# Kernel optimization log

Hardware: AMD Instinct MI355X
Metric: run time of the kernel (lower is better)

The kernel has to match this reference:

```python
import jax, jax.numpy as jnp
import numpy as np

EPS = 1e-5  # torch GroupNorm default


def setup_inputs() -> dict:
    key = jax.random.key(0)
    ks = jax.random.split(key, 7)
    B, H, W, C = 8, 64, 64, 64
    x = jax.random.normal(ks[0], (B, H, W, C), dtype=jnp.float32)
    temb = jax.random.normal(ks[1], (B, 256), dtype=jnp.float32)
    scale = 0.02
    Wq = jax.random.normal(ks[2], (C, C), dtype=jnp.float32) * scale
    Wk = jax.random.normal(ks[3], (C, C), dtype=jnp.float32) * scale
    Wv = jax.random.normal(ks[4], (C, C), dtype=jnp.float32) * scale
    Wo = jax.random.normal(ks[5], (C, C), dtype=jnp.float32) * scale
    z = jnp.zeros((C,), dtype=jnp.float32)
    return {"x": x, "temb": temb, "Wq": Wq, "bq": z, "Wk": Wk, "bk": z,
            "Wv": Wv, "bv": z, "Wo": Wo, "bo": z}


def reference(x, temb, Wq, bq, Wk, bk, Wv, bv, Wo, bo):
    # x: [B, H, W, C] channels-last. temb is accepted but unused (as in source).
    B, H, W, C = x.shape
    S = H * W
    # normalize(): freshly-built GroupNorm(num_groups=1) with identity affine
    # -> standardize over all non-batch dims.
    mu = jnp.mean(x, axis=(1, 2, 3), keepdims=True)
    var = jnp.var(x, axis=(1, 2, 3), keepdims=True)
    h = (x - mu) * jax.lax.rsqrt(var + EPS)
    hf = h.reshape(B, S, C)
    q = hf @ Wq.T + bq  # [B, S, C]
    k = hf @ Wk.T + bk
    v = hf @ Wv.T + bv
    # full (S x S) score matrix, scaled by C^-0.5, naive softmax
    w = jnp.einsum('bsc,btc->bst', q, k) * (C ** -0.5)
    w = jax.nn.softmax(w, axis=-1)
    o = jnp.einsum('bst,btc->bsc', w, v)  # [B, S, C]
    o = o @ Wo.T + bo
    return x + o.reshape(B, H, W, C)
```

## Files before the change

kernel.cpp:

```cpp
#include <hip/hip_runtime.h>
#include <hip/hip_bf16.h>
#include <math.h>

#define B_ 8
#define S_ 4096
#define C_ 64
#define EPSV 1e-5f

using floatx4 = __attribute__((ext_vector_type(4))) float;
using bf16x8  = __attribute__((ext_vector_type(8))) short;
using bf16x4  = __attribute__((ext_vector_type(4))) short;

typedef __attribute__((address_space(3))) unsigned int       as3_u32;
typedef __attribute__((address_space(1))) const unsigned int as1_u32;

__device__ __forceinline__ short f2bf(float f) {
    unsigned u = __builtin_bit_cast(unsigned, f);
    u = u + 0x7fffu + ((u >> 16) & 1u);
    return (short)(u >> 16);
}

__device__ __forceinline__ float bf2f(short s) {
    return __builtin_bit_cast(float, ((unsigned)(unsigned short)s) << 16);
}

__device__ __forceinline__ unsigned cvt_pk_bf16(float lo, float hi) {
    unsigned r;
    asm volatile("v_cvt_pk_bf16_f32 %0, %1, %2" : "=v"(r) : "v"(lo), "v"(hi));
    return r;
}

__device__ __forceinline__ floatx4 mfma_16x16x16_bf16(bf16x4 a, bf16x4 b, floatx4 c) {
#if __has_builtin(__builtin_amdgcn_mfma_f32_16x16x16bf16_1k)
    return __builtin_amdgcn_mfma_f32_16x16x16bf16_1k(a, b, c, 0, 0, 0);
#else
    asm("v_mfma_f32_16x16x16_bf16 %0, %1, %2, %0" : "+v"(c) : "v"(a), "v"(b));
    return c;
#endif
}

__device__ __forceinline__ bf16x8 ld_w_frag(const float* __restrict__ W, int n, int kk, int g, int c) {
    const float* p = W + (16 * n + c) * C_ + 32 * kk + 8 * g;
    bf16x8 r;
#pragma unroll
    for (int j = 0; j < 8; ++j) r[j] = f2bf(p[j]);
    return r;
}

__global__ __launch_bounds__(256) void stats1_kernel(const float* __restrict__ x,
                                                     float* __restrict__ partial) {
    int b = blockIdx.x >> 5, chunk = blockIdx.x & 31;
    const float4* xb = (const float4*)x + (size_t)b * 65536 + chunk * 2048;
    float s = 0.f, ss = 0.f;
#pragma unroll
    for (int i = 0; i < 8; ++i) {
        float4 v = xb[threadIdx.x + i * 256];
        s  += v.x + v.y + v.z + v.w;
        ss += v.x * v.x + v.y * v.y + v.z * v.z + v.w * v.w;
    }
    for (int off = 32; off > 0; off >>= 1) {
        s  += __shfl_down(s, off);
        ss += __shfl_down(ss, off);
    }
    __shared__ float sm[4], ssm[4];
    int wid = threadIdx.x >> 6, lane = threadIdx.x & 63;
    if (lane == 0) { sm[wid] = s; ssm[wid] = ss; }
    __syncthreads();
    if (threadIdx.x == 0) {
        partial[blockIdx.x * 2]     = sm[0] + sm[1] + sm[2] + sm[3];
        partial[blockIdx.x * 2 + 1] = ssm[0] + ssm[1] + ssm[2] + ssm[3];
    }
}

__global__ __launch_bounds__(512) void stats2_kernel(const float* __restrict__ partial,
                                                     float* __restrict__ stats) {
    int w = threadIdx.x >> 6, lane = threadIdx.x & 63;
    float s = 0.f, ss = 0.f;
    if (lane < 32) {
        s  = partial[(w * 32 + lane) * 2];
        ss = partial[(w * 32 + lane) * 2 + 1];
    }
    for (int off = 16; off > 0; off >>= 1) {
        s  += __shfl_down(s, off);
        ss += __shfl_down(ss, off);
    }
    if (lane == 0) {
        const float invN = 1.0f / (float)(S_ * C_);
        float mu  = s * invN;
        float var = ss * invN - mu * mu;
        stats[w * 2]     = mu;
        stats[w * 2 + 1] = rsqrtf(var + EPSV);
    }
}

__global__ __launch_bounds__(256) void proj_kernel(
    const float* __restrict__ x,
    const float* __restrict__ Wq, const float* __restrict__ bq,
    const float* __restrict__ Wk, const float* __restrict__ bk,
    const float* __restrict__ Wv, const float* __restrict__ bv,
    const float* __restrict__ stats,
    short* __restrict__ qo, char* __restrict__ kws, char* __restrict__ vws) {
    __shared__ char hbuf[64 * 128];

    int b  = blockIdx.x >> 6;
    int t_ = blockIdx.x & 63;
    int s0 = t_ * 64;
    float mu = stats[b * 2], rs = stats[b * 2 + 1];
    const float* xt = x + ((size_t)b * S_ + s0) * C_;
    int t = threadIdx.x;

#pragma unroll
    for (int i = 0; i < 4; ++i) {
        int fi  = t + 256 * i;
        int row = fi >> 4;
        int c4  = fi & 15;
        float4 v = *(const float4*)(xt + row * C_ + c4 * 4);
        unsigned lo = (unsigned)(unsigned short)f2bf((v.x - mu) * rs) |
                      ((unsigned)(unsigned short)f2bf((v.y - mu) * rs) << 16);
        unsigned hi = (unsigned)(unsigned short)f2bf((v.z - mu) * rs) |
                      ((unsigned)(unsigned short)f2bf((v.w - mu) * rs) << 16);
        int off = row * 128 + c4 * 8;
        off ^= (row & 7) << 4;
        *(uint2*)(hbuf + off) = make_uint2(lo, hi);
    }
    __syncthreads();

    int lane = t & 63, w = t >> 6;
    int g = lane >> 4, c = lane & 15;

    auto ld_h = [&](int row, int kcol) -> bf16x8 {
        int off = row * 128 + kcol * 2;
        off ^= (row & 7) << 4;
        return *(const bf16x8*)(hbuf + off);
    };

    bf16x8 ha[2];
    ha[0] = ld_h(16 * w + c, 8 * g);
    ha[1] = ld_h(16 * w + c, 32 + 8 * g);

    const float QSC = 0.125f * 1.44269504088896340736f;

#pragma unroll
    for (int n = 0; n < 4; ++n) {
        floatx4 aq = {0.f, 0.f, 0.f, 0.f}, ak = {0.f, 0.f, 0.f, 0.f};
#pragma unroll
        for (int kk = 0; kk < 2; ++kk) {
            bf16x8 wq = ld_w_frag(Wq, n, kk, g, c);
            bf16x8 wk = ld_w_frag(Wk, n, kk, g, c);
            aq = __builtin_amdgcn_mfma_f32_16x16x32_bf16(ha[kk], wq, aq, 0, 0, 0);
            ak = __builtin_amdgcn_mfma_f32_16x16x32_bf16(ha[kk], wk, ak, 0, 0, 0);
        }
        float bqv = bq[16 * n + c], bkv = bk[16 * n + c];
#pragma unroll
        for (int r = 0; r < 4; ++r) {
            int rr = 16 * w + 4 * g + r;
            qo[((size_t)b * S_ + s0 + rr) * C_ + 16 * n + c] = f2bf((aq[r] + bqv) * QSC);
            int r32 = rr & 31;
            size_t tb = ((size_t)b * 128 + 2 * t_ + (rr >> 5)) * 4096;
            int koff = (r32 * 128 + (16 * n + c) * 2) ^ ((r32 & 7) << 4);
            *(short*)(kws + tb + koff) = f2bf(ak[r] + bkv);
        }
    }

    bf16x8 wv[2];
    wv[0] = ld_w_frag(Wv, w, 0, g, c);
    wv[1] = ld_w_frag(Wv, w, 1, g, c);
    float bvr[4];
#pragma unroll
    for (int r = 0; r < 4; ++r) bvr[r] = bv[16 * w + 4 * g + r];

#pragma unroll
    for (int n = 0; n < 4; ++n) {
        floatx4 av = {0.f, 0.f, 0.f, 0.f};
#pragma unroll
        for (int kk = 0; kk < 2; ++kk) {
            bf16x8 hb = ld_h(16 * n + c, 32 * kk + 8 * g);
            av = __builtin_amdgcn_mfma_f32_16x16x32_bf16(wv[kk], hb, av, 0, 0, 0);
        }
        int u   = 16 * n + c;
        int u32 = u & 31;
        size_t tb = ((size_t)b * 128 + 2 * t_ + (u >> 5)) * 4096;
#pragma unroll
        for (int r = 0; r < 4; ++r) {
            int rr = 16 * w + 4 * g + r;
            int voff = (rr * 64 + u32 * 2) ^ ((rr & 7) << 3);
            *(short*)(vws + tb + voff) = f2bf(av[r] + bvr[r]);
        }
    }
}

__global__ __launch_bounds__(256, 8) void flash_kernel(
    const short* __restrict__ qm, const char* __restrict__ kws, const char* __restrict__ vws,
    short* __restrict__ Opart, float2* __restrict__ mlpart) {
    __shared__ char lds[16384];

    int bid = blockIdx.x;
    int logical = (bid & 7) * 256 + (bid >> 3);
    int b = logical >> 8;
    int rest = logical & 255;
    int q0 = (rest >> 2) * 64;
    int quarter = rest & 3;
    int t = threadIdx.x;
    int lane = t & 63, w = t >> 6;
    int g = lane >> 4, c = lane & 15;
    int qw = q0 + 16 * w;

    const char* kbase = kws + (size_t)b * 128 * 4096;
    const char* vbase = vws + (size_t)b * 128 * 4096;
    const short* qp = qm + (size_t)b * S_ * C_;

    bf16x8 bqf[2];
    bqf[0] = *(const bf16x8*)(qp + (qw + c) * C_ + 8 * g);
    bqf[1] = *(const bf16x8*)(qp + (qw + c) * C_ + 32 + 8 * g);

    floatx4 oacc[4];
#pragma unroll
    for (int n = 0; n < 4; ++n) oacc[n] = (floatx4){0.f, 0.f, 0.f, 0.f};
    float m = -__builtin_inff(), lsum = 0.f;

    const int xmask  = (c & 7) << 4;
    const int vxmask = (c & 7) << 3;

    auto STAGE = [&](int bi, int tt) {
        const char* gk = kbase + (size_t)tt * 4096 + t * 16;
        const char* gv = vbase + (size_t)tt * 4096 + t * 16;
        char* lk = lds +        bi * 4096 + t * 16;
        char* lv = lds + 8192 + bi * 4096 + t * 16;
        __builtin_amdgcn_global_load_lds((as1_u32*)gk, (as3_u32*)lk, 16, 0, 0);
        __builtin_amdgcn_global_load_lds((as1_u32*)gv, (as3_u32*)lv, 16, 0, 0);
    };

    auto ld_k = [&](const char* buf, int s, int colb) -> bf16x8 {
        return *(const bf16x8*)(buf + s * 2048 + c * 128 + (colb ^ xmask));
    };
    auto ld_v = [&](const char* buf, int mi, int s) -> bf16x4 {
        return *(const bf16x4*)(buf + mi * 1024 + c * 64 + ((32 * s + 8 * g) ^ vxmask));
    };

    auto COMPUTE = [&](int bi) {
        const char* kbuf = lds +        bi * 4096;
        const char* vbuf = lds + 8192 + bi * 4096;
        floatx4 st[2];
        __builtin_amdgcn_s_setprio(1);
#pragma unroll
        for (int s = 0; s < 2; ++s) {
            st[s] = (floatx4){0.f, 0.f, 0.f, 0.f};
#pragma unroll
            for (int kk = 0; kk < 2; ++kk) {
                bf16x8 ak = ld_k(kbuf, s, 64 * kk + 16 * g);
                st[s] = __builtin_amdgcn_mfma_f32_16x16x32_bf16(ak, bqf[kk], st[s], 0, 0, 0);
            }
        }
        __builtin_amdgcn_s_setprio(0);
        float mt = st[0][0];
#pragma unroll
        for (int s = 0; s < 2; ++s)
#pragma unroll
            for (int r = 0; r < 4; ++r) mt = fmaxf(mt, st[s][r]);
        mt = fmaxf(mt, __shfl_xor(mt, 16));
        mt = fmaxf(mt, __shfl_xor(mt, 32));
        if (!__all(mt - m <= 8.0f)) {
            float mnew  = fmaxf(m, mt);
            float alpha = __builtin_amdgcn_exp2f(m - mnew);
            lsum *= alpha;
            m = mnew;
#pragma unroll
            for (int n = 0; n < 4; ++n) oacc[n] *= alpha;
        }
        bf16x4 pb[2];
        float psum = 0.f;
#pragma unroll
        for (int s = 0; s < 2; ++s) {
            float e0 = __builtin_amdgcn_exp2f(st[s][0] - m);
            float e1 = __builtin_amdgcn_exp2f(st[s][1] - m);
            float e2 = __builtin_amdgcn_exp2f(st[s][2] - m);
            float e3 = __builtin_amdgcn_exp2f(st[s][3] - m);
            psum += (e0 + e1) + (e2 + e3);
            uint2 u = make_uint2(cvt_pk_bf16(e0, e1), cvt_pk_bf16(e2, e3));
            pb[s] = __builtin_bit_cast(bf16x4, u);
        }
        lsum += psum;
        __builtin_amdgcn_s_setprio(1);
#pragma unroll
        for (int s = 0; s < 2; ++s) {
#pragma unroll
            for (int mi = 0; mi < 4; ++mi) {
                bf16x4 av = ld_v(vbuf, mi, s);
                oacc[mi] = mfma_16x16x16_bf16(av, pb[s], oacc[mi]);
            }
        }
        __builtin_amdgcn_s_setprio(0);
    };

    const int base = quarter * 32;
    STAGE(0, base);
    __syncthreads();
    for (int r = 0; r < 32; r += 2) {
        STAGE(1, base + r + 1);
        COMPUTE(0);
        __syncthreads();
        if (r + 2 < 32) STAGE(0, base + r + 2);
        COMPUTE(1);
        __syncthreads();
    }

    lsum += __shfl_xor(lsum, 16);
    lsum += __shfl_xor(lsum, 32);

    size_t prow = (size_t)(quarter * 8 + b) * S_ + q0;
    if (lane < 16)
        mlpart[prow + 16 * w + lane] = make_float2(m, lsum);

    short* op = Opart + (prow + 16 * w + c) * C_;
#pragma unroll
    for (int mi = 0; mi < 4; ++mi) {
        uint2 u = make_uint2(cvt_pk_bf16(oacc[mi][0], oacc[mi][1]),
                             cvt_pk_bf16(oacc[mi][2], oacc[mi][3]));
        *(uint2*)(op + 16 * mi + 4 * g) = u;
    }
}

__global__ __launch_bounds__(256) void combine_kernel(
    const short* __restrict__ Opart, const float2* __restrict__ mlpart,
    const float* __restrict__ Wo, const float* __restrict__ bo,
    const float* __restrict__ x, float* __restrict__ out) {
    __shared__ char obuf[8192];

    int bid = blockIdx.x;
    int logical = (bid & 7) * 64 + (bid >> 3);
    int b = logical >> 6;
    int q0 = (logical & 63) * 64;
    int t = threadIdx.x;
    int lane = t & 63, w = t >> 6;
    int g = lane >> 4, c = lane & 15;

    const short*  P[4];
    const float2* ml[4];
#pragma unroll
    for (int h = 0; h < 4; ++h) {
        P[h]  = Opart  + ((size_t)(h * 8 + b) * S_ + q0) * C_;
        ml[h] = mlpart + (size_t)(h * 8 + b) * S_ + q0;
    }

#pragma unroll
    for (int i = 0; i < 16; ++i) {
        int idx = t + 256 * i;
        int q = idx >> 6, ch = idx & 63;
        float2 a0 = ml[0][q], a1 = ml[1][q], a2 = ml[2][q], a3 = ml[3][q];
        float M = fmaxf(fmaxf(a0.x, a1.x), fmaxf(a2.x, a3.x));
        float s0 = __builtin_amdgcn_exp2f(a0.x - M);
        float s1 = __builtin_amdgcn_exp2f(a1.x - M);
        float s2 = __builtin_amdgcn_exp2f(a2.x - M);
        float s3 = __builtin_amdgcn_exp2f(a3.x - M);
        float L  = a0.y * s0 + a1.y * s1 + a2.y * s2 + a3.y * s3;
        float o  = (bf2f(P[0][q * 64 + ch]) * s0 + bf2f(P[1][q * 64 + ch]) * s1 +
                    bf2f(P[2][q * 64 + ch]) * s2 + bf2f(P[3][q * 64 + ch]) * s3) / L;
        int off = (q * 128 + ch * 2) ^ ((q & 7) << 4);
        *(short*)(obuf + off) = f2bf(o);
    }
    __syncthreads();

    bf16x8 ao[2];
    {
        int row = 16 * w + c;
        int off0 = (row * 128 + (8 * g) * 2)      ^ ((row & 7) << 4);
        int off1 = (row * 128 + (32 + 8 * g) * 2) ^ ((row & 7) << 4);
        ao[0] = *(const bf16x8*)(obuf + off0);
        ao[1] = *(const bf16x8*)(obuf + off1);
    }
#pragma unroll
    for (int n = 0; n < 4; ++n) {
        floatx4 a = {0.f, 0.f, 0.f, 0.f};
#pragma unroll
        for (int kk = 0; kk < 2; ++kk) {
            bf16x8 bw = ld_w_frag(Wo, n, kk, g, c);
            a = __builtin_amdgcn_mfma_f32_16x16x32_bf16(ao[kk], bw, a, 0, 0, 0);
        }
        float bov = bo[16 * n + c];
#pragma unroll
        for (int r = 0; r < 4; ++r) {
            int srow = q0 + 16 * w + 4 * g + r;
            size_t idx = ((size_t)b * S_ + srow) * C_ + 16 * n + c;
            out[idx] = x[idx] + bov + a[r];
        }
    }
}

extern "C" void kernel_launch(void* const* d_in, const int* in_sizes, int n_in,
                              void* d_out, int out_size, void* d_ws, size_t ws_size,
                              hipStream_t stream) {
    const float* x  = (const float*)d_in[0];
    const float* Wq = (const float*)d_in[2];
    const float* bq = (const float*)d_in[3];
    const float* Wk = (const float*)d_in[4];
    const float* bk = (const float*)d_in[5];
    const float* Wv = (const float*)d_in[6];
    const float* bv = (const float*)d_in[7];
    const float* Wo = (const float*)d_in[8];
    const float* bo = (const float*)d_in[9];
    float* out = (float*)d_out;

    char* ws = (char*)d_ws;
    float*  partial = (float*)ws;
    float*  stats   = (float*)(ws + 2048);
    short*  q   = (short*)(ws + 4096);
    char*   kt  = (char*)(q + (size_t)B_ * S_ * C_);
    char*   vt  = kt + (size_t)B_ * 128 * 4096;
    short*  op  = (short*)(vt + (size_t)B_ * 128 * 4096);
    float2* mlp = (float2*)((char*)op + (size_t)4 * B_ * S_ * C_ * 2);

    stats1_kernel<<<256, 256, 0, stream>>>(x, partial);
    stats2_kernel<<<1, 512, 0, stream>>>(partial, stats);
    proj_kernel<<<B_ * (S_ / 64), 256, 0, stream>>>(x, Wq, bq, Wk, bk, Wv, bv, stats, q, kt, vt);
    flash_kernel<<<B_ * (S_ / 64) * 4, 256, 0, stream>>>(q, kt, vt, op, mlp);
    combine_kernel<<<B_ * (S_ / 64), 256, 0, stream>>>(op, mlp, Wo, bo, x, out);
}
```

Measured before the change: 93.74 us.

## Process two query tiles per wave to reuse staged K/V fragments

Each wave now handles 32 query rows (two 16-row tiles) instead of 16, so every block covers 128 queries and the grid is halved. K and V fragments loaded from LDS are read once into registers and reused for both query tiles, halving LDS reads and global K/V staging per query. The cost is roughly double the accumulator and score registers, with launch bounds lowered to 4 waves per SIMD, which may reduce occupancy and latency hiding.

```diff
diff --git a/kernel.cpp b/kernel.cpp
--- a/kernel.cpp
+++ b/kernel.cpp
@@ -189,34 +189,39 @@
     }
 }
 
-__global__ __launch_bounds__(256, 8) void flash_kernel(
+__global__ __launch_bounds__(256, 4) void flash_kernel(
     const short* __restrict__ qm, const char* __restrict__ kws, const char* __restrict__ vws,
     short* __restrict__ Opart, float2* __restrict__ mlpart) {
     __shared__ char lds[16384];
 
     int bid = blockIdx.x;
-    int logical = (bid & 7) * 256 + (bid >> 3);
-    int b = logical >> 8;
-    int rest = logical & 255;
-    int q0 = (rest >> 2) * 64;
+    int logical = (bid & 7) * 128 + (bid >> 3);
+    int b = logical >> 7;
+    int rest = logical & 127;
+    int q0 = (rest >> 2) * 128;
     int quarter = rest & 3;
     int t = threadIdx.x;
     int lane = t & 63, w = t >> 6;
     int g = lane >> 4, c = lane & 15;
-    int qw = q0 + 16 * w;
+    int qw = q0 + 32 * w;
 
     const char* kbase = kws + (size_t)b * 128 * 4096;
     const char* vbase = vws + (size_t)b * 128 * 4096;
     const short* qp = qm + (size_t)b * S_ * C_;
 
-    bf16x8 bqf[2];
-    bqf[0] = *(const bf16x8*)(qp + (qw + c) * C_ + 8 * g);
-    bqf[1] = *(const bf16x8*)(qp + (qw + c) * C_ + 32 + 8 * g);
-
-    floatx4 oacc[4];
-#pragma unroll
-    for (int n = 0; n < 4; ++n) oacc[n] = (floatx4){0.f, 0.f, 0.f, 0.f};
-    float m = -__builtin_inff(), lsum = 0.f;
+    bf16x8 bqf[2][2];
+#pragma unroll
+    for (int qi = 0; qi < 2; ++qi) {
+        bqf[qi][0] = *(const bf16x8*)(qp + (qw + 16 * qi + c) * C_ + 8 * g);
+        bqf[qi][1] = *(const bf16x8*)(qp + (qw + 16 * qi + c) * C_ + 32 + 8 * g);
+    }
+
+    floatx4 oacc[2][4];
+#pragma unroll
+    for (int qi = 0; qi < 2; ++qi)
+#pragma unroll
+        for (int mi = 0; mi < 4; ++mi) oacc[qi][mi] = (floatx4){0.f, 0.f, 0.f, 0.f};
+    float m[2] = {-__builtin_inff(), -__builtin_inff()}, l[2] = {0.f, 0.f};
 
     const int xmask  = (c & 7) << 4;
     const int vxmask = (c & 7) << 3;
@@ -240,55 +245,74 @@
     auto COMPUTE = [&](int bi) {
         const char* kbuf = lds +        bi * 4096;
         const char* vbuf = lds + 8192 + bi * 4096;
-        floatx4 st[2];
+        bf16x8 ak[2][2];
+#pragma unroll
+        for (int s = 0; s < 2; ++s)
+#pragma unroll
+            for (int kk = 0; kk < 2; ++kk)
+                ak[s][kk] = ld_k(kbuf, s, 64 * kk + 16 * g);
+        floatx4 st[2][2];
         __builtin_amdgcn_s_setprio(1);
 #pragma unroll
-        for (int s = 0; s < 2; ++s) {
-            st[s] = (floatx4){0.f, 0.f, 0.f, 0.f};
-#pragma unroll
-            for (int kk = 0; kk < 2; ++kk) {
-                bf16x8 ak = ld_k(kbuf, s, 64 * kk + 16 * g);
-                st[s] = __builtin_amdgcn_mfma_f32_16x16x32_bf16(ak, bqf[kk], st[s], 0, 0, 0);
+        for (int qi = 0; qi < 2; ++qi)
+#pragma unroll
+            for (int s = 0; s < 2; ++s) {
+                st[qi][s] = (floatx4){0.f, 0.f, 0.f, 0.f};
+                st[qi][s] = __builtin_amdgcn_mfma_f32_16x16x32_bf16(ak[s][0], bqf[qi][0], st[qi][s], 0, 0, 0);
+                st[qi][s] = __builtin_amdgcn_mfma_f32_16x16x32_bf16(ak[s][1], bqf[qi][1], st[qi][s], 0, 0, 0);
             }
-        }
         __builtin_amdgcn_s_setprio(0);
-        float mt = st[0][0];
+        bf16x4 av[2][4];
 #pragma unroll
         for (int s = 0; s < 2; ++s)
 #pragma unroll
-            for (int r = 0; r < 4; ++r) mt = fmaxf(mt, st[s][r]);
-        mt = fmaxf(mt, __shfl_xor(mt, 16));
-        mt = fmaxf(mt, __shfl_xor(mt, 32));
-        if (!__all(mt - m <= 8.0f)) {
-            float mnew  = fmaxf(m, mt);
-            float alpha = __builtin_amdgcn_exp2f(m - mnew);
-            lsum *= alpha;
-            m = mnew;
-#pragma unroll
-            for (int n = 0; n < 4; ++n) oacc[n] *= alpha;
-        }
-        bf16x4 pb[2];
-        float psum = 0.f;
-#pragma unroll
-        for (int s = 0; s < 2; ++s) {
-            float e0 = __builtin_amdgcn_exp2f(st[s][0] - m);
-            float e1 = __builtin_amdgcn_exp2f(st[s][1] - m);
-            float e2 = __builtin_amdgcn_exp2f(st[s][2] - m);
-            float e3 = __builtin_amdgcn_exp2f(st[s][3] - m);
-            psum += (e0 + e1) + (e2 + e3);
-            uint2 u = make_uint2(cvt_pk_bf16(e0, e1), cvt_pk_bf16(e2, e3));
-            pb[s] = __builtin_bit_cast(bf16x4, u);
-        }
-        lsum += psum;
+            for (int mi = 0; mi < 4; ++mi)
+                av[s][mi] = ld_v(vbuf, mi, s);
+        float mt[2], need = -1e30f;
+#pragma unroll
+        for (int qi = 0; qi < 2; ++qi) {
+            float v = fmaxf(fmaxf(st[qi][0][0], st[qi][0][1]), fmaxf(st[qi][0][2], st[qi][0][3]));
+            v = fmaxf(v, fmaxf(fmaxf(st[qi][1][0], st[qi][1][1]), fmaxf(st[qi][1][2], st[qi][1][3])));
+            v = fmaxf(v, __shfl_xor(v, 16));
+            v = fmaxf(v, __shfl_xor(v, 32));
+            mt[qi] = v;
+            need = fmaxf(need, v - m[qi]);
+        }
+        if (!__all(need <= 8.0f)) {
+#pragma unroll
+            for (int qi = 0; qi < 2; ++qi) {
+                float mn = fmaxf(m[qi], mt[qi]);
+                float a  = __builtin_amdgcn_exp2f(m[qi] - mn);
+                m[qi] = mn;
+                l[qi] *= a;
+#pragma unroll
+                for (int mi = 0; mi < 4; ++mi) oacc[qi][mi] *= a;
+            }
+        }
+        bf16x4 pb[2][2];
+#pragma unroll
+        for (int qi = 0; qi < 2; ++qi) {
+            float psum = 0.f;
+#pragma unroll
+            for (int s = 0; s < 2; ++s) {
+                float e0 = __builtin_amdgcn_exp2f(st[qi][s][0] - m[qi]);
+                float e1 = __builtin_amdgcn_exp2f(st[qi][s][1] - m[qi]);
+                float e2 = __builtin_amdgcn_exp2f(st[qi][s][2] - m[qi]);
+                float e3 = __builtin_amdgcn_exp2f(st[qi][s][3] - m[qi]);
+                psum += (e0 + e1) + (e2 + e3);
+                uint2 u = make_uint2(cvt_pk_bf16(e0, e1), cvt_pk_bf16(e2, e3));
+                pb[qi][s] = __builtin_bit_cast(bf16x4, u);
+            }
+            l[qi] += psum;
+        }
         __builtin_amdgcn_s_setprio(1);
 #pragma unroll
-        for (int s = 0; s < 2; ++s) {
-#pragma unroll
-            for (int mi = 0; mi < 4; ++mi) {
-                bf16x4 av = ld_v(vbuf, mi, s);
-                oacc[mi] = mfma_16x16x16_bf16(av, pb[s], oacc[mi]);
-            }
-        }
+        for (int qi = 0; qi < 2; ++qi)
+#pragma unroll
+            for (int s = 0; s < 2; ++s)
+#pragma unroll
+                for (int mi = 0; mi < 4; ++mi)
+                    oacc[qi][mi] = mfma_16x16x16_bf16(av[s][mi], pb[qi][s], oacc[qi][mi]);
         __builtin_amdgcn_s_setprio(0);
     };
 
@@ -304,19 +328,28 @@
         __syncthreads();
     }
 
-    lsum += __shfl_xor(lsum, 16);
-    lsum += __shfl_xor(lsum, 32);
+#pragma unroll
+    for (int qi = 0; qi < 2; ++qi) {
+        l[qi] += __shfl_xor(l[qi], 16);
+        l[qi] += __shfl_xor(l[qi], 32);
+    }
 
     size_t prow = (size_t)(quarter * 8 + b) * S_ + q0;
-    if (lane < 16)
-        mlpart[prow + 16 * w + lane] = make_float2(m, lsum);
-
-    short* op = Opart + (prow + 16 * w + c) * C_;
-#pragma unroll
-    for (int mi = 0; mi < 4; ++mi) {
-        uint2 u = make_uint2(cvt_pk_bf16(oacc[mi][0], oacc[mi][1]),
-                             cvt_pk_bf16(oacc[mi][2], oacc[mi][3]));
-        *(uint2*)(op + 16 * mi + 4 * g) = u;
+    if (lane < 16) {
+#pragma unroll
+        for (int qi = 0; qi < 2; ++qi)
+            mlpart[prow + 32 * w + 16 * qi + lane] = make_float2(m[qi], l[qi]);
+    }
+
+#pragma unroll
+    for (int qi = 0; qi < 2; ++qi) {
+        short* op = Opart + (prow + 32 * w + 16 * qi + c) * C_;
+#pragma unroll
+        for (int mi = 0; mi < 4; ++mi) {
+            uint2 u = make_uint2(cvt_pk_bf16(oacc[qi][mi][0], oacc[qi][mi][1]),
+                                 cvt_pk_bf16(oacc[qi][mi][2], oacc[qi][mi][3]));
+            *(uint2*)(op + 16 * mi + 4 * g) = u;
+        }
     }
 }
 
@@ -412,6 +445,6 @@
     stats1_kernel<<<256, 256, 0, stream>>>(x, partial);
     stats2_kernel<<<1, 512, 0, stream>>>(partial, stats);
     proj_kernel<<<B_ * (S_ / 64), 256, 0, stream>>>(x, Wq, bq, Wk, bk, Wv, bv, stats, q, kt, vt);
-    flash_kernel<<<B_ * (S_ / 64) * 4, 256, 0, stream>>>(q, kt, vt, op, mlp);
+    flash_kernel<<<B_ * (S_ / 128) * 4, 256, 0, stream>>>(q, kt, vt, op, mlp);
     combine_kernel<<<B_ * (S_ / 64), 256, 0, stream>>>(op, mlp, Wo, bo, x, out);
 }
```

After: 88.32 us. 5.8% less time.

## Switch flash attention to 32x32x16 MFMA with 128-query blocks

Applied to the files above, without the earlier changes.

The flash kernel now gives each wave 32 query rows and uses 32x32x16 bf16 MFMAs for both QK^T and PV instead of 16x16 tiles, so each staged K/V tile is reused across twice as many queries. The probability tile is rearranged in registers with permlane32 swaps rather than shuffles, and the running max is folded into the MFMA accumulator's initial value so the exp needs no separate subtraction. The V swizzle in the projection kernel changes to match the new LDS read pattern. The grid is halved and launch bounds drop to 4 blocks per SIMD, which lowers occupancy and raises register pressure.

```diff
diff --git a/kernel.cpp b/kernel.cpp
--- a/kernel.cpp
+++ b/kernel.cpp
@@ -7,9 +7,9 @@
 #define C_ 64
 #define EPSV 1e-5f
 
-using floatx4 = __attribute__((ext_vector_type(4))) float;
-using bf16x8  = __attribute__((ext_vector_type(8))) short;
-using bf16x4  = __attribute__((ext_vector_type(4))) short;
+using floatx4  = __attribute__((ext_vector_type(4)))  float;
+using floatx16 = __attribute__((ext_vector_type(16))) float;
+using bf16x8   = __attribute__((ext_vector_type(8)))  short;
 
 typedef __attribute__((address_space(3))) unsigned int       as3_u32;
 typedef __attribute__((address_space(1))) const unsigned int as1_u32;
@@ -30,12 +30,13 @@
     return r;
 }
 
-__device__ __forceinline__ floatx4 mfma_16x16x16_bf16(bf16x4 a, bf16x4 b, floatx4 c) {
-#if __has_builtin(__builtin_amdgcn_mfma_f32_16x16x16bf16_1k)
-    return __builtin_amdgcn_mfma_f32_16x16x16bf16_1k(a, b, c, 0, 0, 0);
+__device__ __forceinline__ void perm32swap(unsigned &a, unsigned &b) {
+#if __has_builtin(__builtin_amdgcn_permlane32_swap)
+    auto r = __builtin_amdgcn_permlane32_swap((int)a, (int)b, false, false);
+    a = (unsigned)r[0];
+    b = (unsigned)r[1];
 #else
-    asm("v_mfma_f32_16x16x16_bf16 %0, %1, %2, %0" : "+v"(c) : "v"(a), "v"(b));
-    return c;
+    asm volatile("v_permlane32_swap_b32 %0, %1" : "+v"(a), "+v"(b));
 #endif
 }
 
@@ -183,43 +184,46 @@
 #pragma unroll
         for (int r = 0; r < 4; ++r) {
             int rr = 16 * w + 4 * g + r;
-            int voff = (rr * 64 + u32 * 2) ^ ((rr & 7) << 3);
+            int voff = (rr * 64 + u32 * 2) ^ (((rr >> 1) & 3) << 4);
             *(short*)(vws + tb + voff) = f2bf(av[r] + bvr[r]);
         }
     }
 }
 
-__global__ __launch_bounds__(256, 8) void flash_kernel(
+__global__ __launch_bounds__(256, 4) void flash_kernel(
     const short* __restrict__ qm, const char* __restrict__ kws, const char* __restrict__ vws,
     short* __restrict__ Opart, float2* __restrict__ mlpart) {
     __shared__ char lds[16384];
 
     int bid = blockIdx.x;
-    int logical = (bid & 7) * 256 + (bid >> 3);
-    int b = logical >> 8;
-    int rest = logical & 255;
-    int q0 = (rest >> 2) * 64;
+    int logical = (bid & 7) * 128 + (bid >> 3);
+    int b = logical >> 7;
+    int rest = logical & 127;
+    int q0 = (rest >> 2) * 128;
     int quarter = rest & 3;
     int t = threadIdx.x;
     int lane = t & 63, w = t >> 6;
-    int g = lane >> 4, c = lane & 15;
-    int qw = q0 + 16 * w;
+    int r5 = lane & 31, hi = lane >> 5;
+    int qw = q0 + 32 * w;
 
     const char* kbase = kws + (size_t)b * 128 * 4096;
     const char* vbase = vws + (size_t)b * 128 * 4096;
     const short* qp = qm + (size_t)b * S_ * C_;
 
-    bf16x8 bqf[2];
-    bqf[0] = *(const bf16x8*)(qp + (qw + c) * C_ + 8 * g);
-    bqf[1] = *(const bf16x8*)(qp + (qw + c) * C_ + 32 + 8 * g);
-
-    floatx4 oacc[4];
-#pragma unroll
-    for (int n = 0; n < 4; ++n) oacc[n] = (floatx4){0.f, 0.f, 0.f, 0.f};
-    float m = -__builtin_inff(), lsum = 0.f;
-
-    const int xmask  = (c & 7) << 4;
-    const int vxmask = (c & 7) << 3;
+    bf16x8 bq[4];
+#pragma unroll
+    for (int kk = 0; kk < 4; ++kk)
+        bq[kk] = *(const bf16x8*)(qp + (qw + r5) * C_ + 16 * kk + 8 * hi);
+
+    floatx16 oacc[2];
+#pragma unroll
+    for (int mm = 0; mm < 2; ++mm)
+#pragma unroll
+        for (int i = 0; i < 16; ++i) oacc[mm][i] = 0.f;
+    float m = -64.f, nm = 64.f, l = 0.f;
+
+    const int kxm = (r5 & 7) << 4;
+    const int vxm = ((r5 >> 1) & 3) << 4;
 
     auto STAGE = [&](int bi, int tt) {
         const char* gk = kbase + (size_t)tt * 4096 + t * 16;
@@ -230,64 +234,69 @@
         __builtin_amdgcn_global_load_lds((as1_u32*)gv, (as3_u32*)lv, 16, 0, 0);
     };
 
-    auto ld_k = [&](const char* buf, int s, int colb) -> bf16x8 {
-        return *(const bf16x8*)(buf + s * 2048 + c * 128 + (colb ^ xmask));
+    auto ld_k = [&](const char* buf, int kk) -> bf16x8 {
+        return *(const bf16x8*)(buf + r5 * 128 + ((32 * kk + 16 * hi) ^ kxm));
     };
-    auto ld_v = [&](const char* buf, int mi, int s) -> bf16x4 {
-        return *(const bf16x4*)(buf + mi * 1024 + c * 64 + ((32 * s + 8 * g) ^ vxmask));
+    auto ld_v = [&](const char* buf, int mm, int s) -> bf16x8 {
+        return *(const bf16x8*)(buf + (32 * mm + r5) * 64 + ((32 * s + 16 * hi) ^ vxm));
     };
 
     auto COMPUTE = [&](int bi) {
         const char* kbuf = lds +        bi * 4096;
         const char* vbuf = lds + 8192 + bi * 4096;
-        floatx4 st[2];
+        floatx16 st;
+#pragma unroll
+        for (int i = 0; i < 16; ++i) st[i] = nm;
         __builtin_amdgcn_s_setprio(1);
 #pragma unroll
-        for (int s = 0; s < 2; ++s) {
-            st[s] = (floatx4){0.f, 0.f, 0.f, 0.f};
-#pragma unroll
-            for (int kk = 0; kk < 2; ++kk) {
-                bf16x8 ak = ld_k(kbuf, s, 64 * kk + 16 * g);
-                st[s] = __builtin_amdgcn_mfma_f32_16x16x32_bf16(ak, bqf[kk], st[s], 0, 0, 0);
-            }
+        for (int kk = 0; kk < 4; ++kk) {
+            bf16x8 ak = ld_k(kbuf, kk);
+            st = __builtin_amdgcn_mfma_f32_32x32x16_bf16(ak, bq[kk], st, 0, 0, 0);
         }
         __builtin_amdgcn_s_setprio(0);
-        float mt = st[0][0];
-#pragma unroll
-        for (int s = 0; s < 2; ++s)
-#pragma unroll
-            for (int r = 0; r < 4; ++r) mt = fmaxf(mt, st[s][r]);
-        mt = fmaxf(mt, __shfl_xor(mt, 16));
+        bf16x8 av[2][2];
+#pragma unroll
+        for (int mm = 0; mm < 2; ++mm)
+#pragma unroll
+            for (int s = 0; s < 2; ++s)
+                av[mm][s] = ld_v(vbuf, mm, s);
+        float mt = st[0];
+#pragma unroll
+        for (int i = 1; i < 16; ++i) mt = fmaxf(mt, st[i]);
         mt = fmaxf(mt, __shfl_xor(mt, 32));
-        if (!__all(mt - m <= 8.0f)) {
-            float mnew  = fmaxf(m, mt);
-            float alpha = __builtin_amdgcn_exp2f(m - mnew);
-            lsum *= alpha;
-            m = mnew;
-#pragma unroll
-            for (int n = 0; n < 4; ++n) oacc[n] *= alpha;
-        }
-        bf16x4 pb[2];
-        float psum = 0.f;
-#pragma unroll
-        for (int s = 0; s < 2; ++s) {
-            float e0 = __builtin_amdgcn_exp2f(st[s][0] - m);
-            float e1 = __builtin_amdgcn_exp2f(st[s][1] - m);
-            float e2 = __builtin_amdgcn_exp2f(st[s][2] - m);
-            float e3 = __builtin_amdgcn_exp2f(st[s][3] - m);
-            psum += (e0 + e1) + (e2 + e3);
-            uint2 u = make_uint2(cvt_pk_bf16(e0, e1), cvt_pk_bf16(e2, e3));
-            pb[s] = __builtin_bit_cast(bf16x4, u);
-        }
-        lsum += psum;
+        if (!__all(mt <= 8.0f)) {
+            float d = fmaxf(mt, 0.f);
+            float a = __builtin_amdgcn_exp2f(-d);
+            m += d;
+            nm = -m;
+            l *= a;
+#pragma unroll
+            for (int mm = 0; mm < 2; ++mm) oacc[mm] *= a;
+#pragma unroll
+            for (int i = 0; i < 16; ++i) st[i] -= d;
+        }
+        float e[16], psum = 0.f;
+#pragma unroll
+        for (int i = 0; i < 16; ++i) e[i] = __builtin_amdgcn_exp2f(st[i]);
+#pragma unroll
+        for (int i = 0; i < 16; ++i) psum += e[i];
+        l += psum;
+        unsigned wd[8];
+#pragma unroll
+        for (int j = 0; j < 8; ++j) wd[j] = cvt_pk_bf16(e[2 * j], e[2 * j + 1]);
+        perm32swap(wd[0], wd[2]);
+        perm32swap(wd[1], wd[3]);
+        perm32swap(wd[4], wd[6]);
+        perm32swap(wd[5], wd[7]);
+        uint4 u0 = make_uint4(wd[0], wd[1], wd[2], wd[3]);
+        uint4 u1 = make_uint4(wd[4], wd[5], wd[6], wd[7]);
+        bf16x8 bp0 = __builtin_bit_cast(bf16x8, u0);
+        bf16x8 bp1 = __builtin_bit_cast(bf16x8, u1);
         __builtin_amdgcn_s_setprio(1);
 #pragma unroll
-        for (int s = 0; s < 2; ++s) {
-#pragma unroll
-            for (int mi = 0; mi < 4; ++mi) {
-                bf16x4 av = ld_v(vbuf, mi, s);
-                oacc[mi] = mfma_16x16x16_bf16(av, pb[s], oacc[mi]);
-            }
+        for (int mm = 0; mm < 2; ++mm) {
+            oacc[mm] = __builtin_amdgcn_mfma_f32_32x32x16_bf16(av[mm][0], bp0, oacc[mm], 0, 0, 0);
+            oacc[mm] = __builtin_amdgcn_mfma_f32_32x32x16_bf16(av[mm][1], bp1, oacc[mm], 0, 0, 0);
         }
         __builtin_amdgcn_s_setprio(0);
     };
@@ -304,19 +313,22 @@
         __syncthreads();
     }
 
-    lsum += __shfl_xor(lsum, 16);
-    lsum += __shfl_xor(lsum, 32);
+    l += __shfl_xor(l, 32);
 
     size_t prow = (size_t)(quarter * 8 + b) * S_ + q0;
-    if (lane < 16)
-        mlpart[prow + 16 * w + lane] = make_float2(m, lsum);
-
-    short* op = Opart + (prow + 16 * w + c) * C_;
-#pragma unroll
-    for (int mi = 0; mi < 4; ++mi) {
-        uint2 u = make_uint2(cvt_pk_bf16(oacc[mi][0], oacc[mi][1]),
-                             cvt_pk_bf16(oacc[mi][2], oacc[mi][3]));
-        *(uint2*)(op + 16 * mi + 4 * g) = u;
+    if (lane < 32)
+        mlpart[prow + 32 * w + r5] = make_float2(m, l);
+
+    short* op = Opart + (prow + 32 * w + r5) * C_;
+#pragma unroll
+    for (int mm = 0; mm < 2; ++mm) {
+#pragma unroll
+        for (int j = 0; j < 4; ++j) {
+            int ch = 32 * mm + 8 * j + 4 * hi;
+            uint2 u = make_uint2(cvt_pk_bf16(oacc[mm][4 * j],     oacc[mm][4 * j + 1]),
+                                 cvt_pk_bf16(oacc[mm][4 * j + 2], oacc[mm][4 * j + 3]));
+            *(uint2*)(op + ch) = u;
+        }
     }
 }
 
@@ -412,6 +424,6 @@
     stats1_kernel<<<256, 256, 0, stream>>>(x, partial);
     stats2_kernel<<<1, 512, 0, stream>>>(partial, stats);
     proj_kernel<<<B_ * (S_ / 64), 256, 0, stream>>>(x, Wq, bq, Wk, bk, Wv, bv, stats, q, kt, vt);
-    flash_kernel<<<B_ * (S_ / 64) * 4, 256, 0, stream>>>(q, kt, vt, op, mlp);
+    flash_kernel<<<B_ * (S_ / 128) * 4, 256, 0, stream>>>(q, kt, vt, op, mlp);
     combine_kernel<<<B_ * (S_ / 64), 256, 0, stream>>>(op, mlp, Wo, bo, x, out);
 }
```

Measured after the change: 80.69 us. 1.16x faster.
